# Optimization experiments

Hardware: AMD Instinct MI355X
Metric: run time of the kernel (lower is better)

Reference implementation:

```python
import jax, jax.numpy as jnp
import numpy as np
from jax import lax

NEG = -1e30  # safe -inf surrogate (avoids inf-inf NaNs under vjp)


def setup_inputs() -> dict:
    key = jax.random.key(0)
    k1, k2, k3, k4 = jax.random.split(key, 4)
    B, T, U, V = 8, 128, 64, 1024
    acts = jax.random.normal(k1, (B, T, U + 1, V), dtype=jnp.float32)
    # labels in [1, V): blank (0) never appears in target sequences
    labels = jax.random.randint(k2, (B, U), 1, V, dtype=jnp.int32)
    act_lens = jax.random.randint(k3, (B,), T // 2, T + 1, dtype=jnp.int32)
    label_lens = jax.random.randint(k4, (B,), U // 2, U + 1, dtype=jnp.int32)
    return {"acts": acts, "labels": labels, "act_lens": act_lens, "label_lens": label_lens}


def _rnnt_costs(acts, labels, act_lens, label_lens, blank=0):
    """Per-example negative log-likelihood of the RNNT alignment lattice.
    acts: (B, T, U+1, V) logits (warp_rnnt applies log_softmax internally).
    """
    B, T, U1, V = acts.shape
    U = U1 - 1
    lp = jax.nn.log_softmax(acts, axis=-1)
    lp_blank = lp[..., blank]                                        # (B, T, U+1)
    lab = jnp.broadcast_to(labels[:, None, :, None], (B, T, U, 1))
    lp_label = jnp.take_along_axis(lp[:, :, :U, :], lab, axis=3)[..., 0]  # (B, T, U)
    # mask label emissions beyond each example's label length
    umask = jnp.arange(U)[None, :] < label_lens[:, None]             # (B, U)
    lp_label = jnp.where(umask[:, None, :], lp_label, NEG)

    def compute_row(fb, lt):
        # fb: (B, U+1) alpha[t-1, u] + lp_blank[t-1, u] (the "from below" term)
        # lt: (B, U)   label log-probs at time t
        # new[u] = logaddexp(fb[u], new[u-1] + lt[u-1])  -- sequential in u
        def u_step(carry, x):
            fb_u, lt_u = x
            new = jnp.logaddexp(fb_u, carry + lt_u)
            return new, new
        _, rest = lax.scan(u_step, fb[:, 0], (fb[:, 1:].T, lt.T))    # (U, B)
        return jnp.concatenate([fb[:, 0:1], rest.T], axis=1)         # (B, U+1)

    # t = 0 row: alpha[0,0] = 0; only label transitions along u
    fb0 = jnp.concatenate([jnp.zeros((B, 1), acts.dtype), jnp.full((B, U), NEG, acts.dtype)], axis=1)
    row0 = compute_row(fb0, lp_label[:, 0, :])

    def t_step(prev_row, x):
        lpb_prev, lt = x
        row = compute_row(prev_row + lpb_prev, lt)
        return row, row

    xs = (jnp.moveaxis(lp_blank[:, :-1, :], 0, 1),   # (T-1, B, U+1)
          jnp.moveaxis(lp_label[:, 1:, :], 0, 1))    # (T-1, B, U)
    _, rows = lax.scan(t_step, row0, xs)             # (T-1, B, U+1)
    alphas = jnp.concatenate([row0[None], rows], axis=0)  # (T, B, U+1)

    b = jnp.arange(B)
    tl = act_lens - 1
    final = alphas[tl, b, label_lens] + lp_blank[b, tl, label_lens]
    return -final                                     # (B,)


def reference(acts, labels, act_lens, label_lens):
    # matches torch module defaults: size_average=False, blank_label=0
    costs = _rnnt_costs(acts, labels, act_lens, label_lens, blank=0)
    return jnp.sum(costs).reshape(1)
```

## Files before the change

kernel.cpp:

```cpp
#include <hip/hip_runtime.h>

#define NEGF (-1e30f)
#define INV_LN2 1.4426950408889634f
#define LN2F    0.6931471805599453f

#define B_   8
#define T_   128
#define U_   64
#define U1_  65
#define V_   1024
#define PAD_ 66
#define ROWS_ (B_*T_*U1_)
#define WS_PER_ (T_*PAD_)

typedef float f32x4 __attribute__((ext_vector_type(4)));

__device__ __forceinline__ float wave_shr1(float x) {
  return __int_as_float(__builtin_amdgcn_update_dpp(
      __float_as_int(x), __float_as_int(x), 0x138, 0xf, 0xf, 0));
}

__global__ __launch_bounds__(256) void k1_logsoftmax(
    const float* __restrict__ acts, const int* __restrict__ labels,
    const int* __restrict__ label_lens,
    float* __restrict__ lpb, float* __restrict__ lpl, int* __restrict__ cnt) {
  const int lane = threadIdx.x & 63;
  const int wv   = threadIdx.x >> 6;
  const int row  = blockIdx.x * 4 + wv;

  if (blockIdx.x == 0 && threadIdx.x == 0) *cnt = 0;

  const int b   = row / (T_ * U1_);
  const int rem = row - b * (T_ * U1_);
  const int t   = rem / U1_;
  const int u   = rem - t * U1_;

  const float* __restrict__ p = acts + (size_t)row * V_;

  int ll_ = 0; float labv = 0.0f;
  if (lane == 0 && u < U_) {
    ll_  = label_lens[b];
    labv = p[labels[b * U_ + u]];
  }

  f32x4 v0 = *(const f32x4*)(p +   0 + lane * 4);
  f32x4 v1 = *(const f32x4*)(p + 256 + lane * 4);
  f32x4 v2 = *(const f32x4*)(p + 512 + lane * 4);
  f32x4 v3 = *(const f32x4*)(p + 768 + lane * 4);

  float m = fmaxf(fmaxf(fmaxf(v0.x, v0.y), fmaxf(v0.z, v0.w)),
            fmaxf(fmaxf(fmaxf(v1.x, v1.y), fmaxf(v1.z, v1.w)),
            fmaxf(fmaxf(fmaxf(v2.x, v2.y), fmaxf(v2.z, v2.w)),
                  fmaxf(fmaxf(v3.x, v3.y), fmaxf(v3.z, v3.w)))));
  #pragma unroll
  for (int o = 32; o; o >>= 1) m = fmaxf(m, __shfl_xor(m, o, 64));

  float s = __expf(v0.x - m) + __expf(v0.y - m) + __expf(v0.z - m) + __expf(v0.w - m)
          + __expf(v1.x - m) + __expf(v1.y - m) + __expf(v1.z - m) + __expf(v1.w - m)
          + __expf(v2.x - m) + __expf(v2.y - m) + __expf(v2.z - m) + __expf(v2.w - m)
          + __expf(v3.x - m) + __expf(v3.y - m) + __expf(v3.z - m) + __expf(v3.w - m);
  #pragma unroll
  for (int o = 32; o; o >>= 1) s += __shfl_xor(s, o, 64);

  float lse = m + __logf(s);

  if (lane == 0) {
    int base = (b * T_ + t) * PAD_;
    lpb[base + u] = (v0.x - lse) * INV_LN2;
    if (u < U_) lpl[base + u] = (u < ll_) ? ((labv - lse) * INV_LN2) : NEGF;
  }
}

__global__ __launch_bounds__(256) void k2_alpha(
    const float* __restrict__ lpb, const float* __restrict__ lpl,
    const int* __restrict__ act_lens, const int* __restrict__ label_lens,
    float* __restrict__ costs, int* __restrict__ cnt, float* __restrict__ out) {
  __shared__ float lpb_s[WS_PER_];
  __shared__ float lpl_s[WS_PER_];
  __shared__ float alpha0_s[256];
  const int b = blockIdx.x;

  {
    const f32x4* s1 = (const f32x4*)(lpb + (size_t)b * WS_PER_);
    const f32x4* s2 = (const f32x4*)(lpl + (size_t)b * WS_PER_);
    f32x4* d1 = (f32x4*)lpb_s;
    f32x4* d2 = (f32x4*)lpl_s;
    #pragma unroll
    for (int k = 0; k < 9; ++k) {
      int i = k * 256 + (int)threadIdx.x;
      if (i < WS_PER_ / 4) { d1[i] = s1[i]; d2[i] = s2[i]; }
    }
  }
  __syncthreads();
  if (threadIdx.x >= 64) return;

  const int l  = threadIdx.x;
  const int tl = act_lens[b] - 1;
  const int ll = label_lens[b];

  float x0 = lpb_s[l * PAD_];
  float x1 = lpb_s[(l + 64) * PAD_];
  float s0 = x0;
  #pragma unroll
  for (int o = 1; o < 64; o <<= 1) { float tmp = __shfl_up(s0, o, 64); if (l >= o) s0 += tmp; }
  float tot0 = __shfl(s0, 63, 64);
  float s1v = x1;
  #pragma unroll
  for (int o = 1; o < 64; o <<= 1) { float tmp = __shfl_up(s1v, o, 64); if (l >= o) s1v += tmp; }
  alpha0_s[l]      = s0 - x0;
  alpha0_s[l + 64] = tot0 + s1v - x1;
  alpha0_s[128 + l] = NEGF;
  if (l < 64) alpha0_s[192 + l] = NEGF;

  const int u    = l + 1;
  const bool isme = (u == ll);
  float a    = NEGF;
  float fin  = 0.0f;
  bool  have = false;

  int ipb = u;
  int ipl = u - 1;
  int ia0 = 0;

  float pb0 = lpb_s[ipb], pl0 = lpl_s[ipl], pa00 = alpha0_s[ia0];
  ipb += (1 > u)  ? PAD_ : 0;
  ipl += (1 >= u) ? PAD_ : 0;
  ia0  = 1;
  float pb1 = lpb_s[ipb], pl1 = lpl_s[ipl], pa01 = alpha0_s[ia0];
  ipb += (2 > u)  ? PAD_ : 0;
  ipl += (2 >= u) ? PAD_ : 0;
  ia0  = 2;

#define STEP_(DD, PB, PL, PA0) do {                                   \
    int  t_ = (DD) - u;                                               \
    float left = wave_shr1(a);                                        \
    if (l == 0) left = (PA0);                                         \
    float blank = a + (PB);          \
    float label = left + (PL);                                        \
    float mx = fmaxf(blank, label);                                   \
    float mn = fminf(blank, label);                                   \
    float e_; asm("v_exp_f32 %0, %1" : "=v"(e_) : "v"(mn - mx));      \
    float g_; asm("v_log_f32 %0, %1" : "=v"(g_) : "v"(1.0f + e_));    \
    float anew = mx + g_;                                             \
    bool valid = (t_ >= 0) && (t_ < T_);                              \
    a = valid ? anew : NEGF;                                          \
    if (isme && t_ == tl) { fin = a; have = true; }                   \
  } while (0)

  #pragma unroll 1
  for (int d = 1; d <= T_ - 1 + U_; d += 2) {
    float nb0 = lpb_s[ipb], nl0 = lpl_s[ipl], na00 = alpha0_s[ia0];
    ipb += (d + 2 > u)  ? PAD_ : 0;
    ipl += (d + 2 >= u) ? PAD_ : 0;
    ++ia0;
    STEP_(d, pb0, pl0, pa00);
    float nb1 = lpb_s[ipb], nl1 = lpl_s[ipl], na01 = alpha0_s[ia0];
    ipb += (d + 3 > u)  ? PAD_ : 0;
    ipl += (d + 3 >= u) ? PAD_ : 0;
    ++ia0;
    STEP_(d + 1, pb1, pl1, pa01);

    pb0 = nb0; pl0 = nl0; pa00 = na00;
    pb1 = nb1; pl1 = nl1; pa01 = na01;
  }
#undef STEP_

  if (have)              costs[b] = -(fin + lpb_s[tl * PAD_ + ll]) * LN2F;
  if (l == 0 && ll == 0) costs[b] = -(alpha0_s[tl] + lpb_s[tl * PAD_]) * LN2F;

  __threadfence();
  if (l == 0) {
    int old = atomicAdd(cnt, 1);
    if (old == B_ - 1) {
      __threadfence();
      volatile const float* vc = costs;
      float s = 0.0f;
      #pragma unroll
      for (int i = 0; i < B_; ++i) s += vc[i];
      out[0] = s;
    }
  }
}

extern "C" void kernel_launch(void* const* d_in, const int* in_sizes, int n_in,
                              void* d_out, int out_size, void* d_ws, size_t ws_size,
                              hipStream_t stream) {
  const float* acts       = (const float*)d_in[0];
  const int*   labels     = (const int*)d_in[1];
  const int*   act_lens   = (const int*)d_in[2];
  const int*   label_lens = (const int*)d_in[3];

  float* lpb   = (float*)d_ws;
  float* lpl   = lpb + (size_t)B_ * WS_PER_;
  float* costs = lpl + (size_t)B_ * WS_PER_;
  int*   cnt   = (int*)(costs + B_);

  k1_logsoftmax<<<ROWS_ / 4, 256, 0, stream>>>(acts, labels, label_lens, lpb, lpl, cnt);
  k2_alpha<<<B_, 256, 0, stream>>>(lpb, lpl, act_lens, label_lens, costs, cnt, (float*)d_out);
}
```

Before: 66.74 us.

## Fuse log-softmax and alpha recursion into one kernel with per-slab flag pipelining

The two kernels are merged into a single launch. The first 8 blocks run the alpha recursion and spin on per-(t,b) completion counters, while the remaining blocks compute log-softmax rows and write blank and label log-probs into a diagonal-major packed float2 layout. This lets the sequential alpha scan overlap with the bandwidth-bound softmax pass, removes the shared-memory staging step, and replaces the prefix-sum setup with a running sum. In exchange it adds a memset, spin-wait polling, and a dependence on the 8 consumer blocks being scheduled before the producers, which could deadlock or stall if scheduling order differs.

```diff
diff --git a/kernel.cpp b/kernel.cpp
--- a/kernel.cpp
+++ b/kernel.cpp
@@ -9,9 +9,13 @@
 #define U_   64
 #define U1_  65
 #define V_   1024
-#define PAD_ 66
-#define ROWS_ (B_*T_*U1_)
-#define WS_PER_ (T_*PAD_)
+#define NDIAG_ 208
+#define DS_    66
+#define PACKB_ (NDIAG_*DS_)
+#define SLABS_ (T_*B_)
+#define BPS_   17
+#define K1_BLOCKS_ (SLABS_*BPS_)
+#define WPS_   (BPS_*4)
 
 typedef float f32x4 __attribute__((ext_vector_type(4)));
 
@@ -20,163 +24,161 @@
       __float_as_int(x), __float_as_int(x), 0x138, 0xf, 0xf, 0));
 }
 
-__global__ __launch_bounds__(256) void k1_logsoftmax(
+__global__ __launch_bounds__(256) void rnnt_all(
     const float* __restrict__ acts, const int* __restrict__ labels,
-    const int* __restrict__ label_lens,
-    float* __restrict__ lpb, float* __restrict__ lpl, int* __restrict__ cnt) {
-  const int lane = threadIdx.x & 63;
-  const int wv   = threadIdx.x >> 6;
-  const int row  = blockIdx.x * 4 + wv;
-
-  if (blockIdx.x == 0 && threadIdx.x == 0) *cnt = 0;
-
-  const int b   = row / (T_ * U1_);
-  const int rem = row - b * (T_ * U1_);
-  const int t   = rem / U1_;
-  const int u   = rem - t * U1_;
-
-  const float* __restrict__ p = acts + (size_t)row * V_;
-
-  int ll_ = 0; float labv = 0.0f;
-  if (lane == 0 && u < U_) {
-    ll_  = label_lens[b];
-    labv = p[labels[b * U_ + u]];
-  }
-
-  f32x4 v0 = *(const f32x4*)(p +   0 + lane * 4);
-  f32x4 v1 = *(const f32x4*)(p + 256 + lane * 4);
-  f32x4 v2 = *(const f32x4*)(p + 512 + lane * 4);
-  f32x4 v3 = *(const f32x4*)(p + 768 + lane * 4);
-
-  float m = fmaxf(fmaxf(fmaxf(v0.x, v0.y), fmaxf(v0.z, v0.w)),
-            fmaxf(fmaxf(fmaxf(v1.x, v1.y), fmaxf(v1.z, v1.w)),
-            fmaxf(fmaxf(fmaxf(v2.x, v2.y), fmaxf(v2.z, v2.w)),
-                  fmaxf(fmaxf(v3.x, v3.y), fmaxf(v3.z, v3.w)))));
-  #pragma unroll
-  for (int o = 32; o; o >>= 1) m = fmaxf(m, __shfl_xor(m, o, 64));
-
-  float s = __expf(v0.x - m) + __expf(v0.y - m) + __expf(v0.z - m) + __expf(v0.w - m)
-          + __expf(v1.x - m) + __expf(v1.y - m) + __expf(v1.z - m) + __expf(v1.w - m)
-          + __expf(v2.x - m) + __expf(v2.y - m) + __expf(v2.z - m) + __expf(v2.w - m)
-          + __expf(v3.x - m) + __expf(v3.y - m) + __expf(v3.z - m) + __expf(v3.w - m);
-  #pragma unroll
-  for (int o = 32; o; o >>= 1) s += __shfl_xor(s, o, 64);
-
-  float lse = m + __logf(s);
-
-  if (lane == 0) {
-    int base = (b * T_ + t) * PAD_;
-    lpb[base + u] = (v0.x - lse) * INV_LN2;
-    if (u < U_) lpl[base + u] = (u < ll_) ? ((labv - lse) * INV_LN2) : NEGF;
-  }
-}
-
-__global__ __launch_bounds__(256) void k2_alpha(
-    const float* __restrict__ lpb, const float* __restrict__ lpl,
     const int* __restrict__ act_lens, const int* __restrict__ label_lens,
-    float* __restrict__ costs, int* __restrict__ cnt, float* __restrict__ out) {
-  __shared__ float lpb_s[WS_PER_];
-  __shared__ float lpl_s[WS_PER_];
-  __shared__ float alpha0_s[256];
-  const int b = blockIdx.x;
-
-  {
-    const f32x4* s1 = (const f32x4*)(lpb + (size_t)b * WS_PER_);
-    const f32x4* s2 = (const f32x4*)(lpl + (size_t)b * WS_PER_);
-    f32x4* d1 = (f32x4*)lpb_s;
-    f32x4* d2 = (f32x4*)lpl_s;
-    #pragma unroll
-    for (int k = 0; k < 9; ++k) {
-      int i = k * 256 + (int)threadIdx.x;
-      if (i < WS_PER_ / 4) { d1[i] = s1[i]; d2[i] = s2[i]; }
+    float2* __restrict__ pack, float* __restrict__ costs,
+    int* __restrict__ cnt, int* __restrict__ done, float* __restrict__ out) {
+
+  const int bid = (int)blockIdx.x;
+
+  if (bid >= B_) {
+    const int kb   = bid - B_;
+    const int sid  = kb / BPS_;
+    const int j    = kb - sid * BPS_;
+    const int t    = sid >> 3;
+    const int b    = sid & 7;
+    const int lane = threadIdx.x & 63;
+    const int w    = threadIdx.x >> 6;
+    const int u    = 4 * j + w;
+
+    if (u < U1_) {
+      const float* __restrict__ p =
+          acts + (size_t)((b * T_ + t) * U1_ + u) * V_;
+
+      int ll_ = 0; float labv = 0.0f;
+      if (lane == 0 && u < U_) {
+        ll_  = label_lens[b];
+        labv = p[labels[b * U_ + u]];
+      }
+
+      f32x4 v0 = *(const f32x4*)(p +   0 + lane * 4);
+      f32x4 v1 = *(const f32x4*)(p + 256 + lane * 4);
+      f32x4 v2 = *(const f32x4*)(p + 512 + lane * 4);
+      f32x4 v3 = *(const f32x4*)(p + 768 + lane * 4);
+
+      float m = fmaxf(fmaxf(fmaxf(v0.x, v0.y), fmaxf(v0.z, v0.w)),
+                fmaxf(fmaxf(fmaxf(v1.x, v1.y), fmaxf(v1.z, v1.w)),
+                fmaxf(fmaxf(fmaxf(v2.x, v2.y), fmaxf(v2.z, v2.w)),
+                      fmaxf(fmaxf(v3.x, v3.y), fmaxf(v3.z, v3.w)))));
+      #pragma unroll
+      for (int o = 32; o; o >>= 1) m = fmaxf(m, __shfl_xor(m, o, 64));
+
+      float s = __expf(v0.x - m) + __expf(v0.y - m) + __expf(v0.z - m) + __expf(v0.w - m)
+              + __expf(v1.x - m) + __expf(v1.y - m) + __expf(v1.z - m) + __expf(v1.w - m)
+              + __expf(v2.x - m) + __expf(v2.y - m) + __expf(v2.z - m) + __expf(v2.w - m)
+              + __expf(v3.x - m) + __expf(v3.y - m) + __expf(v3.z - m) + __expf(v3.w - m);
+      #pragma unroll
+      for (int o = 32; o; o >>= 1) s += __shfl_xor(s, o, 64);
+
+      float lse = m + __logf(s);
+
+      if (lane == 0) {
+        float2* pg = pack + (size_t)b * PACKB_ + (size_t)(t + u) * DS_;
+        __hip_atomic_store(&pg[u].x, (v0.x - lse) * INV_LN2,
+                           __ATOMIC_RELAXED, __HIP_MEMORY_SCOPE_AGENT);
+        if (u < U_) {
+          float val = (u < ll_) ? ((labv - lse) * INV_LN2) : NEGF;
+          __hip_atomic_store(&pg[u + 1].y, val,
+                             __ATOMIC_RELAXED, __HIP_MEMORY_SCOPE_AGENT);
+        }
+      }
     }
-  }
-  __syncthreads();
+    if (lane == 0) {
+      asm volatile("s_waitcnt vmcnt(0)" ::: "memory");
+      __hip_atomic_fetch_add(&cnt[sid], 1,
+                             __ATOMIC_RELAXED, __HIP_MEMORY_SCOPE_AGENT);
+    }
+    return;
+  }
+
   if (threadIdx.x >= 64) return;
-
-  const int l  = threadIdx.x;
+  const int l  = (int)threadIdx.x;
+  const int b  = bid;
   const int tl = act_lens[b] - 1;
   const int ll = label_lens[b];
-
-  float x0 = lpb_s[l * PAD_];
-  float x1 = lpb_s[(l + 64) * PAD_];
-  float s0 = x0;
-  #pragma unroll
-  for (int o = 1; o < 64; o <<= 1) { float tmp = __shfl_up(s0, o, 64); if (l >= o) s0 += tmp; }
-  float tot0 = __shfl(s0, 63, 64);
-  float s1v = x1;
-  #pragma unroll
-  for (int o = 1; o < 64; o <<= 1) { float tmp = __shfl_up(s1v, o, 64); if (l >= o) s1v += tmp; }
-  alpha0_s[l]      = s0 - x0;
-  alpha0_s[l + 64] = tot0 + s1v - x1;
-  alpha0_s[128 + l] = NEGF;
-  if (l < 64) alpha0_s[192 + l] = NEGF;
-
-  const int u    = l + 1;
+  const float2* __restrict__ pk = pack + (size_t)b * PACKB_;
+
+  const int  u    = l + 1;
   const bool isme = (u == ll);
-  float a    = NEGF;
-  float fin  = 0.0f;
-  bool  have = false;
-
-  int ipb = u;
-  int ipl = u - 1;
-  int ia0 = 0;
-
-  float pb0 = lpb_s[ipb], pl0 = lpl_s[ipl], pa00 = alpha0_s[ia0];
-  ipb += (1 > u)  ? PAD_ : 0;
-  ipl += (1 >= u) ? PAD_ : 0;
-  ia0  = 1;
-  float pb1 = lpb_s[ipb], pl1 = lpl_s[ipl], pa01 = alpha0_s[ia0];
-  ipb += (2 > u)  ? PAD_ : 0;
-  ipl += (2 >= u) ? PAD_ : 0;
-  ia0  = 2;
-
-#define STEP_(DD, PB, PL, PA0) do {                                   \
-    int  t_ = (DD) - u;                                               \
+  float a      = NEGF;
+  float fin    = 0.0f;
+  float pa0run = 0.0f;
+  float a0cap  = 0.0f, fdcap = 0.0f;
+  int   frontier = 0;
+
+#define WAITTO_(NEED) do {                                                   \
+    int need_ = (NEED); if (need_ > T_ - 1) need_ = T_ - 1;                  \
+    if (frontier <= need_) {                                                 \
+      while (frontier <= need_) {                                            \
+        int c_ = __hip_atomic_load(&cnt[frontier * B_ + b],                  \
+                                   __ATOMIC_RELAXED, __HIP_MEMORY_SCOPE_AGENT); \
+        if (c_ == WPS_) ++frontier; else __builtin_amdgcn_s_sleep(2);        \
+      }                                                                      \
+      __threadfence();                  \
+    }                                                                        \
+  } while (0)
+
+#define STEP_(DC, Q, F) do {                                          \
+    int t_ = (DC) - u;                                                \
     float left = wave_shr1(a);                                        \
-    if (l == 0) left = (PA0);                                         \
-    float blank = a + (PB);          \
-    float label = left + (PL);                                        \
-    float mx = fmaxf(blank, label);                                   \
-    float mn = fminf(blank, label);                                   \
+    left = (l == 0) ? pa0run : left;                                  \
+    float blank  = a + (Q).x;                                         \
+    float labelv = left + (Q).y;                                      \
+    float mx = fmaxf(blank, labelv);                                  \
+    float mn = fminf(blank, labelv);                                  \
     float e_; asm("v_exp_f32 %0, %1" : "=v"(e_) : "v"(mn - mx));      \
     float g_; asm("v_log_f32 %0, %1" : "=v"(g_) : "v"(1.0f + e_));    \
     float anew = mx + g_;                                             \
-    bool valid = (t_ >= 0) && (t_ < T_);                              \
+    bool valid = ((unsigned)t_ < (unsigned)T_);                       \
     a = valid ? anew : NEGF;                                          \
-    if (isme && t_ == tl) { fin = a; have = true; }                   \
+    fin   = (isme && t_ == tl)        ? a      : fin;                 \
+    a0cap = (l == 0 && (DC) == tl + 1) ? pa0run : a0cap;              \
+    fdcap = (l == 0 && (DC) == tl + 1) ? (F)    : fdcap;              \
+    pa0run += (F);                                                    \
   } while (0)
 
+  WAITTO_(15);
+  float2 q0 = pk[0 * DS_ + u], q1 = pk[1 * DS_ + u], q2 = pk[2 * DS_ + u], q3 = pk[3 * DS_ + u];
+  float2 q4 = pk[4 * DS_ + u], q5 = pk[5 * DS_ + u], q6 = pk[6 * DS_ + u], q7 = pk[7 * DS_ + u];
+  float  f0 = pk[0 * DS_].x, f1 = pk[1 * DS_].x, f2 = pk[2 * DS_].x, f3 = pk[3 * DS_].x;
+  float  f4 = pk[4 * DS_].x, f5 = pk[5 * DS_].x, f6 = pk[6 * DS_].x, f7 = pk[7 * DS_].x;
+
   #pragma unroll 1
-  for (int d = 1; d <= T_ - 1 + U_; d += 2) {
-    float nb0 = lpb_s[ipb], nl0 = lpl_s[ipl], na00 = alpha0_s[ia0];
-    ipb += (d + 2 > u)  ? PAD_ : 0;
-    ipl += (d + 2 >= u) ? PAD_ : 0;
-    ++ia0;
-    STEP_(d, pb0, pl0, pa00);
-    float nb1 = lpb_s[ipb], nl1 = lpl_s[ipl], na01 = alpha0_s[ia0];
-    ipb += (d + 3 > u)  ? PAD_ : 0;
-    ipl += (d + 3 >= u) ? PAD_ : 0;
-    ++ia0;
-    STEP_(d + 1, pb1, pl1, pa01);
-
-    pb0 = nb0; pl0 = nl0; pa00 = na00;
-    pb1 = nb1; pl1 = nl1; pa01 = na01;
+  for (int d = 1; d <= 185; d += 8) {
+    WAITTO_(d + 14);
+    const float2* pd = pk + (size_t)(d + 7) * DS_;
+    STEP_(d + 0, q0, f0); q0 = pd[0 * DS_ + u]; f0 = pd[0 * DS_].x;
+    STEP_(d + 1, q1, f1); q1 = pd[1 * DS_ + u]; f1 = pd[1 * DS_].x;
+    STEP_(d + 2, q2, f2); q2 = pd[2 * DS_ + u]; f2 = pd[2 * DS_].x;
+    STEP_(d + 3, q3, f3); q3 = pd[3 * DS_ + u]; f3 = pd[3 * DS_].x;
+    STEP_(d + 4, q4, f4); q4 = pd[4 * DS_ + u]; f4 = pd[4 * DS_].x;
+    STEP_(d + 5, q5, f5); q5 = pd[5 * DS_ + u]; f5 = pd[5 * DS_].x;
+    STEP_(d + 6, q6, f6); q6 = pd[6 * DS_ + u]; f6 = pd[6 * DS_].x;
+    STEP_(d + 7, q7, f7); q7 = pd[7 * DS_ + u]; f7 = pd[7 * DS_].x;
   }
 #undef STEP_
-
-  if (have)              costs[b] = -(fin + lpb_s[tl * PAD_ + ll]) * LN2F;
-  if (l == 0 && ll == 0) costs[b] = -(alpha0_s[tl] + lpb_s[tl * PAD_]) * LN2F;
-
-  __threadfence();
+#undef WAITTO_
+
+  if (isme) {
+    float vlast = pk[(size_t)(tl + ll) * DS_ + ll].x;
+    __hip_atomic_store(&costs[b], -(fin + vlast) * LN2F,
+                       __ATOMIC_RELAXED, __HIP_MEMORY_SCOPE_AGENT);
+  }
+  if (l == 0 && ll == 0) {
+    __hip_atomic_store(&costs[b], -(a0cap + fdcap) * LN2F,
+                       __ATOMIC_RELAXED, __HIP_MEMORY_SCOPE_AGENT);
+  }
+
+  asm volatile("s_waitcnt vmcnt(0)" ::: "memory");
   if (l == 0) {
-    int old = atomicAdd(cnt, 1);
-    if (old == B_ - 1) {
+    int o = __hip_atomic_fetch_add(done, 1, __ATOMIC_RELAXED, __HIP_MEMORY_SCOPE_AGENT);
+    if (o == B_ - 1) {
       __threadfence();
-      volatile const float* vc = costs;
       float s = 0.0f;
       #pragma unroll
-      for (int i = 0; i < B_; ++i) s += vc[i];
+      for (int i = 0; i < B_; ++i)
+        s += __hip_atomic_load(&costs[i], __ATOMIC_RELAXED, __HIP_MEMORY_SCOPE_AGENT);
       out[0] = s;
     }
   }
@@ -190,11 +192,12 @@
   const int*   act_lens   = (const int*)d_in[2];
   const int*   label_lens = (const int*)d_in[3];
 
-  float* lpb   = (float*)d_ws;
-  float* lpl   = lpb + (size_t)B_ * WS_PER_;
-  float* costs = lpl + (size_t)B_ * WS_PER_;
-  int*   cnt   = (int*)(costs + B_);
-
-  k1_logsoftmax<<<ROWS_ / 4, 256, 0, stream>>>(acts, labels, label_lens, lpb, lpl, cnt);
-  k2_alpha<<<B_, 256, 0, stream>>>(lpb, lpl, act_lens, label_lens, costs, cnt, (float*)d_out);
+  float2* pack  = (float2*)d_ws;
+  float*  costs = (float*)(pack + (size_t)B_ * PACKB_);
+  int*    cnt   = (int*)(costs + B_);
+  int*    done  = cnt + SLABS_;
+
+  hipMemsetAsync(cnt, 0, (SLABS_ + 1) * sizeof(int), stream);
+  rnnt_all<<<B_ + K1_BLOCKS_, 256, 0, stream>>>(acts, labels, act_lens, label_lens,
+                                                pack, costs, cnt, done, (float*)d_out);
 }
```

New measurement: 128.9 us. 1.93x slower.
